# Kernel optimization log

Hardware: AMD Instinct MI355X
Metric: run time of the kernel (lower is better)

Reference implementation:

```python
import jax, jax.numpy as jnp
import numpy as np

EPS = float(np.finfo(np.float64).eps)  # np.finfo(float).eps as in torch combine


def setup_inputs() -> dict:
    key = jax.random.key(0)
    ks = jax.random.split(key, 4)
    B, E, D_in, D_h, D_out = 4096, 8, 768, 2048, 768
    return {
        "x": jax.random.normal(ks[0], (B, D_in), dtype=jnp.float32),
        "w_gate": jax.random.normal(ks[1], (D_in, E), dtype=jnp.float32) * 0.02,
        "W1": jax.random.normal(ks[2], (E, D_in, D_h), dtype=jnp.float32) * (1.0 / np.sqrt(D_in)),
        "b1": jnp.zeros((E, D_h), dtype=jnp.float32),
        "W2": jax.random.normal(ks[3], (E, D_h, D_out), dtype=jnp.float32) * (1.0 / np.sqrt(D_h)),
        "b2": jnp.zeros((E, D_out), dtype=jnp.float32),
        "k": 2,
    }


def _cv_squared(v):
    # torch .var() is unbiased (ddof=1)
    return jnp.var(v, ddof=1) / (jnp.mean(v) ** 2 + 1e-10)


def _top_k_gates(logits, k):
    B, E = logits.shape
    top_vals, top_idx = jax.lax.top_k(logits, k)        # [B, k]
    top_gates = jax.nn.softmax(top_vals, axis=1)        # softmax over the k kept logits
    gates = jnp.zeros((B, E), logits.dtype).at[jnp.arange(B)[:, None], top_idx].set(top_gates)
    return gates


def reference(x, w_gate, W1, b1, W2, b2, k):
    # --- gating (eval path: noiseless clean logits, softmax gating) ---
    logits = x @ w_gate                                  # [B, E]
    gates = _top_k_gates(logits, k)                      # [B, E], sparse (k nonzeros/row)
    # --- per-expert MLP: Linear -> gelu -> Linear -> log_softmax ---
    # Dense grouped compute over experts; gate==0 terms contribute nothing in combine.
    h = jax.nn.gelu(jnp.einsum('bi,eih->beh', x, W1) + b1[None])      # [B, E, Dh]
    lo = jax.nn.log_softmax(jnp.einsum('beh,eho->beo', h, W2) + b2[None], axis=-1)  # [B, E, Do]
    # --- combine: exp, weight by gates, scatter-add, eps-clamp, log ---
    combined = jnp.einsum('be,beo->bo', gates, jnp.exp(lo))           # [B, Do]
    y = jnp.log(jnp.where(combined == 0, EPS, combined))
    # --- load-balancing aux loss (eval: load = count of nonzero gates) ---
    importance = gates.sum(0)
    load = (gates > 0).sum(0).astype(jnp.float32)
    loss = 0.01 * (_cv_squared(importance) + _cv_squared(load))
    return y, loss
```

## Files before the change

kernel.cpp:

```cpp
#include <hip/hip_runtime.h>
#include <hip/hip_bf16.h>
#include <math.h>

typedef __hip_bfloat16 bf16;
typedef short v8s __attribute__((ext_vector_type(8)));
typedef float v4f __attribute__((ext_vector_type(4)));

#define B_TOK 4096
#define E_EXP 8
#define D_IN  768
#define D_H   2048
#define D_OUT 768
#define MAXT  72

__device__ __forceinline__ void gl_lds16(const bf16* g, bf16* l) {
  __builtin_amdgcn_global_load_lds(
      (const __attribute__((address_space(1))) unsigned int*)g,
      (__attribute__((address_space(3))) unsigned int*)l, 16, 0, 0);
}

__global__ void gate_cvt_kernel(const float* __restrict__ x, const float* __restrict__ wg,
                                bf16* __restrict__ xb,
                                float* __restrict__ gates, int* __restrict__ tidx) {
  int gt = blockIdx.x * 256 + threadIdx.x;
  int tok = gt >> 6, l = gt & 63;
  const float* xr = x + (size_t)tok * D_IN;
  bf16* xbr = xb + (size_t)tok * D_IN;
  float acc[8] = {0.f,0.f,0.f,0.f,0.f,0.f,0.f,0.f};
  #pragma unroll
  for (int i = 0; i < 3; ++i) {
    int k0 = i * 256 + l * 4;
    float4 v = *(const float4*)(xr + k0);
    union { bf16 h[4]; uint2 u; } pk;
    pk.h[0] = __float2bfloat16(v.x); pk.h[1] = __float2bfloat16(v.y);
    pk.h[2] = __float2bfloat16(v.z); pk.h[3] = __float2bfloat16(v.w);
    *(uint2*)(xbr + k0) = pk.u;
    float xv[4] = {v.x, v.y, v.z, v.w};
    #pragma unroll
    for (int j = 0; j < 4; ++j) {
      const float* wr = wg + (size_t)(k0 + j) * 8;
      float4 w0 = *(const float4*)wr;
      float4 w1 = *(const float4*)(wr + 4);
      acc[0] += xv[j] * w0.x; acc[1] += xv[j] * w0.y;
      acc[2] += xv[j] * w0.z; acc[3] += xv[j] * w0.w;
      acc[4] += xv[j] * w1.x; acc[5] += xv[j] * w1.y;
      acc[6] += xv[j] * w1.z; acc[7] += xv[j] * w1.w;
    }
  }
  #pragma unroll
  for (int d = 1; d < 64; d <<= 1)
    #pragma unroll
    for (int e = 0; e < 8; ++e) acc[e] += __shfl_xor(acc[e], d);
  if (l == 0) {
    int i1 = 0; float v1 = acc[0];
    #pragma unroll
    for (int e = 1; e < 8; ++e) if (acc[e] > v1) { v1 = acc[e]; i1 = e; }
    int i2 = -1; float v2 = -1e30f;
    #pragma unroll
    for (int e = 0; e < 8; ++e) if (e != i1 && acc[e] > v2) { v2 = acc[e]; i2 = e; }
    float ex = __expf(v2 - v1);
    float g1 = 1.f / (1.f + ex), g2 = ex / (1.f + ex);
    gates[2 * tok] = g1; gates[2 * tok + 1] = g2;
    tidx[2 * tok] = i1;  tidx[2 * tok + 1] = i2;
  }
}

__global__ void finalize_kernel(const int* __restrict__ tidx, const float* __restrict__ gates,
                                int* __restrict__ cnt_off, int* __restrict__ row_ids,
                                int* __restrict__ pos, int* __restrict__ tmap,
                                float* __restrict__ loss_out) {
  __shared__ int   hcnt[256][9];
  __shared__ float himp[256][9];
  __shared__ int   tot[8], off[8];
  __shared__ float itot[8];
  int t = threadIdx.x;
  #pragma unroll
  for (int e = 0; e < 8; ++e) { hcnt[t][e] = 0; himp[t][e] = 0.f; }
  __syncthreads();
  for (int i = 0; i < 32; ++i) {
    int idx = t * 32 + i;
    int e = tidx[idx];
    hcnt[t][e] += 1;
    himp[t][e] += gates[idx];
  }
  __syncthreads();
  if (t < 8) {
    int run = 0; float s = 0.f;
    for (int j = 0; j < 256; ++j) {
      int c = hcnt[j][t];
      hcnt[j][t] = run;
      run += c;
      s += himp[j][t];
    }
    tot[t] = run; itot[t] = s;
  }
  __syncthreads();
  if (t == 0) {
    int o = 0;
    float mi = 0.f, ml = 0.f;
    for (int e = 0; e < 8; ++e) {
      off[e] = o; o += tot[e];
      cnt_off[e] = tot[e]; cnt_off[8 + e] = off[e];
      mi += itot[e]; ml += (float)tot[e];
    }
    mi *= 0.125f; ml *= 0.125f;
    float vi = 0.f, vl = 0.f;
    for (int e = 0; e < 8; ++e) {
      float d = itot[e] - mi;        vi += d * d;
      float d2 = (float)tot[e] - ml; vl += d2 * d2;
    }
    vi /= 7.f; vl /= 7.f;
    *loss_out = 0.01f * (vi / (mi * mi + 1e-10f) + vl / (ml * ml + 1e-10f));
    int nt = 0;
    for (int e = 0; e < 8; ++e)
      for (int tt = 0; tt < (tot[e] + 127) >> 7; ++tt) {
        tmap[nt] = e; tmap[MAXT + nt] = tt; ++nt;
      }
    for (; nt < MAXT; ++nt) tmap[nt] = -1;
  }
  __syncthreads();
  for (int i = 0; i < 32; ++i) {
    int idx = t * 32 + i;
    int e = tidx[idx];
    int slot = off[e] + hcnt[t][e];
    hcnt[t][e] += 1;
    row_ids[slot] = idx >> 1;
    pos[idx] = slot;
  }
}

__global__ void transpose_cvt(const float* __restrict__ W, bf16* __restrict__ Wt,
                              int K, int N) {
  __shared__ bf16 tile[64][72];
  int e = blockIdx.z;
  int k0 = blockIdx.y * 64, n0 = blockIdx.x * 64;
  const float* Wp = W + (size_t)e * K * N;
  bf16* Wtp = Wt + (size_t)e * N * K;
  int t = threadIdx.x;
  int cr = t >> 4;
  int cc = (t & 15) * 4;
  #pragma unroll
  for (int p = 0; p < 4; ++p) {
    int kr = cr + p * 16;
    float4 v = *(const float4*)(Wp + (size_t)(k0 + kr) * N + n0 + cc);
    tile[cc + 0][kr] = __float2bfloat16(v.x);
    tile[cc + 1][kr] = __float2bfloat16(v.y);
    tile[cc + 2][kr] = __float2bfloat16(v.z);
    tile[cc + 3][kr] = __float2bfloat16(v.w);
  }
  __syncthreads();
  #pragma unroll
  for (int p = 0; p < 2; ++p) {
    int o = p * 256 + t;
    int n = o >> 3, k8 = (o & 7) * 8;
    v8s val = *(const v8s*)&tile[n][k8];
    *(v8s*)(Wtp + (size_t)(n0 + n) * K + k0 + k8) = val;
  }
}

template<int KDIM, bool GATHER, bool GELU>
__global__ __launch_bounds__(256)
void gemm_mlp(const bf16* __restrict__ Ab, const bf16* __restrict__ Wt,
              const float* __restrict__ bias, bf16* __restrict__ Outb,
              const int* __restrict__ row_ids, const int* __restrict__ cnt_off,
              const int* __restrict__ tmap, const int N) {
  constexpr int BK = 64, BM = 128, BN = 128;
  constexpr int NK = KDIM / BK;
  static_assert(NK % 2 == 0, "NK even");
  __shared__ __align__(16) bf16 lsA0[BM * BK], lsB0[BN * BK];
  __shared__ __align__(16) bf16 lsA1[BM * BK], lsB1[BN * BK];
  const int ti = blockIdx.y;
  const int e = tmap[ti];
  if (e < 0) return;
  const int rowb = tmap[MAXT + ti];
  const int cnt = cnt_off[e];
  const int off = cnt_off[8 + e];
  const int colb = blockIdx.x;
  const int t = (int)threadIdx.x, w = t >> 6, l = t & 63;
  const int cs = (l & 7) ^ (l >> 3);
  const bf16* gA[4];
  const bf16* gB[4];
  #pragma unroll
  for (int it = 0; it < 4; ++it) {
    int rt = (it * 4 + w) * 8 + (l >> 3);
    int r = rowb * BM + rt;
    int rc = r < cnt ? r : cnt - 1;
    long arow = GATHER ? (long)row_ids[off + rc] : (long)(off + rc);
    gA[it] = Ab + arow * (long)KDIM + cs * 8;
  }
  #pragma unroll
  for (int it = 0; it < 4; ++it) {
    int rt = (it * 4 + w) * 8 + (l >> 3);
    gB[it] = Wt + ((size_t)e * N + (size_t)colb * BN + rt) * KDIM + cs * 8;
  }
  v4f acc[4][4] = {};
  const int wm = w >> 1, wn = w & 1;

#define STAGE(lA, lB, k0) do {                                             \
    _Pragma("unroll")                                                      \
    for (int it = 0; it < 4; ++it) gl_lds16(gA[it] + (k0), (lA) + (it * 4 + w) * 512); \
    _Pragma("unroll")                                                      \
    for (int it = 0; it < 4; ++it) gl_lds16(gB[it] + (k0), (lB) + (it * 4 + w) * 512); \
  } while (0)

#define COMPUTE(lA, lB) do {                                               \
    _Pragma("unroll")                                                      \
    for (int kk = 0; kk < 2; ++kk) {                                       \
      v8s af[4], bfr[4];                                                   \
      _Pragma("unroll")                                                    \
      for (int fm = 0; fm < 4; ++fm) {                                     \
        int row = wm * 64 + fm * 16 + (l & 15);                            \
        int cg = kk * 4 + (l >> 4);                                        \
        af[fm] = *(const v8s*)((lA) + row * BK + ((cg ^ (row & 7)) << 3)); \
      }                                                                    \
      _Pragma("unroll")                                                    \
      for (int fn = 0; fn < 4; ++fn) {                                     \
        int row = wn * 64 + fn * 16 + (l & 15);                            \
        int cg = kk * 4 + (l >> 4);                                        \
        bfr[fn] = *(const v8s*)((lB) + row * BK + ((cg ^ (row & 7)) << 3));\
      }                                                                    \
      _Pragma("unroll")                                                    \
      for (int fm = 0; fm < 4; ++fm)                                       \
        _Pragma("unroll")                                                  \
        for (int fn = 0; fn < 4; ++fn)                                     \
          acc[fm][fn] = __builtin_amdgcn_mfma_f32_16x16x32_bf16(af[fm], bfr[fn], acc[fm][fn], 0, 0, 0); \
    }                                                                      \
  } while (0)

  STAGE(lsA0, lsB0, 0);
  __syncthreads();
  #pragma unroll 1
  for (int ks = 0; ks < NK; ks += 2) {
    if (ks + 1 < NK) STAGE(lsA1, lsB1, (ks + 1) * BK);
    COMPUTE(lsA0, lsB0);
    __syncthreads();
    if (ks + 2 < NK) STAGE(lsA0, lsB0, (ks + 2) * BK);
    COMPUTE(lsA1, lsB1);
    __syncthreads();
  }
#undef STAGE
#undef COMPUTE

  const float* bp = bias + (size_t)e * N + (size_t)colb * BN;
  #pragma unroll
  for (int fm = 0; fm < 4; ++fm) {
    int lr0 = wm * 64 + fm * 16 + (l >> 4) * 4;
    #pragma unroll
    for (int fn = 0; fn < 4; ++fn) {
      int lcol = wn * 64 + fn * 16 + (l & 15);
      float bv = bp[lcol];
      #pragma unroll
      for (int q = 0; q < 4; ++q) {
        int lr = lr0 + q;
        int r = rowb * BM + lr;
        if (r < cnt) {
          float v = acc[fm][fn][q] + bv;
          if (GELU) {
            float u = 0.7978845608028654f * (v + 0.044715f * v * v * v);
            float th = 1.f - 2.f / (__expf(2.f * u) + 1.f);
            v = 0.5f * v * (1.f + th);
          }
          Outb[(size_t)(off + r) * N + (size_t)colb * BN + lcol] = __float2bfloat16(v);
        }
      }
    }
  }
}

__global__ void combine_kernel(const bf16* __restrict__ z, const float* __restrict__ gates,
                               const int* __restrict__ pos, float* __restrict__ y) {
  int gt = blockIdx.x * 256 + threadIdx.x;
  int tok = gt >> 6, l = gt & 63;
  if (tok >= B_TOK) return;
  const bf16* z1 = z + (size_t)pos[2 * tok] * D_OUT;
  const bf16* z2 = z + (size_t)pos[2 * tok + 1] * D_OUT;
  float g1 = gates[2 * tok], g2 = gates[2 * tok + 1];
  float a[12], b[12];
  float m1 = -1e30f, m2 = -1e30f;
  #pragma unroll
  for (int i = 0; i < 12; ++i) {
    a[i] = __bfloat162float(z1[l + 64 * i]);
    b[i] = __bfloat162float(z2[l + 64 * i]);
    m1 = fmaxf(m1, a[i]); m2 = fmaxf(m2, b[i]);
  }
  #pragma unroll
  for (int d = 1; d < 64; d <<= 1) {
    m1 = fmaxf(m1, __shfl_xor(m1, d));
    m2 = fmaxf(m2, __shfl_xor(m2, d));
  }
  float s1 = 0.f, s2 = 0.f;
  #pragma unroll
  for (int i = 0; i < 12; ++i) { s1 += __expf(a[i] - m1); s2 += __expf(b[i] - m2); }
  #pragma unroll
  for (int d = 1; d < 64; d <<= 1) { s1 += __shfl_xor(s1, d); s2 += __shfl_xor(s2, d); }
  float c1 = g1 / s1, c2 = g2 / s2;
  #pragma unroll
  for (int i = 0; i < 12; ++i) {
    float cmb = c1 * __expf(a[i] - m1) + c2 * __expf(b[i] - m2);
    y[(size_t)tok * D_OUT + l + 64 * i] = logf(cmb == 0.f ? 2.2204460492503131e-16f : cmb);
  }
}

extern "C" void kernel_launch(void* const* d_in, const int* in_sizes, int n_in,
                              void* d_out, int out_size, void* d_ws, size_t ws_size,
                              hipStream_t stream) {
  const float* x  = (const float*)d_in[0];
  const float* wg = (const float*)d_in[1];
  const float* W1 = (const float*)d_in[2];
  const float* b1 = (const float*)d_in[3];
  const float* W2 = (const float*)d_in[4];
  const float* b2 = (const float*)d_in[5];
  float* out = (float*)d_out;

  char* ws = (char*)d_ws;
  int*   cnt_off = (int*)(ws + 0);
  float* gates   = (float*)(ws + 256);
  int*   tidx    = (int*)(ws + 256 + 32768);
  int*   pos     = (int*)(ws + 256 + 65536);
  int*   row_ids = (int*)(ws + 256 + 98304);
  int*   tmap    = (int*)(ws + 256 + 131072);
  const size_t base = 262144;
  bf16* x_bf = (bf16*)(ws + base);
  bf16* W1t  = (bf16*)(ws + base + 6291456);
  bf16* W2t  = (bf16*)(ws + base + 31457280);
  bf16* h_bf = (bf16*)(ws + base + 56623104);
  bf16* z_bf = (bf16*)(ws + base);

  transpose_cvt<<<dim3(D_H / 64,  D_IN / 64, E_EXP), 256, 0, stream>>>(W1, W1t, D_IN, D_H);
  transpose_cvt<<<dim3(D_OUT / 64, D_H / 64, E_EXP), 256, 0, stream>>>(W2, W2t, D_H, D_OUT);
  gate_cvt_kernel<<<dim3(1024), 256, 0, stream>>>(x, wg, x_bf, gates, tidx);
  finalize_kernel<<<dim3(1), 256, 0, stream>>>(tidx, gates, cnt_off, row_ids, pos, tmap,
                                               out + (size_t)B_TOK * D_OUT);
  gemm_mlp<D_IN, true,  true ><<<dim3(D_H / 128,  MAXT), 256, 0, stream>>>(
      x_bf, W1t, b1, h_bf, row_ids, cnt_off, tmap, D_H);
  gemm_mlp<D_H,  false, false><<<dim3(D_OUT / 128, MAXT), 256, 0, stream>>>(
      h_bf, W2t, b2, z_bf, row_ids, cnt_off, tmap, D_OUT);
  combine_kernel<<<dim3(1024), 256, 0, stream>>>(z_bf, gates, pos, out);
}
```

Before: 181.0 us.

## Deepen GEMM pipeline to four LDS stages and vectorize epilogue via LDS

Replaces the double-buffered K loop with a four-buffer ring that keeps three tiles of global-to-LDS loads in flight, using explicit vmcnt waits and raw barriers instead of __syncthreads. The epilogue now stages each warp's accumulators through LDS so each lane writes 8 contiguous bf16 values as one 16-byte store instead of scattered 2-byte stores. It aims to hide global load latency and cut store transactions. In exchange it doubles LDS use to 128 KB per block, which lowers occupancy, and depends on hand-tuned wait counts being correct.

```diff
diff --git a/kernel.cpp b/kernel.cpp
--- a/kernel.cpp
+++ b/kernel.cpp
@@ -166,9 +166,8 @@
               const int* __restrict__ tmap, const int N) {
   constexpr int BK = 64, BM = 128, BN = 128;
   constexpr int NK = KDIM / BK;
-  static_assert(NK % 2 == 0, "NK even");
-  __shared__ __align__(16) bf16 lsA0[BM * BK], lsB0[BN * BK];
-  __shared__ __align__(16) bf16 lsA1[BM * BK], lsB1[BN * BK];
+  static_assert(NK % 4 == 0, "NK multiple of 4");
+  __shared__ __align__(16) bf16 lds[4][2][BM * BK];
   const int ti = blockIdx.y;
   const int e = tmap[ti];
   if (e < 0) return;
@@ -196,72 +195,96 @@
   v4f acc[4][4] = {};
   const int wm = w >> 1, wn = w & 1;
 
-#define STAGE(lA, lB, k0) do {                                             \
-    _Pragma("unroll")                                                      \
-    for (int it = 0; it < 4; ++it) gl_lds16(gA[it] + (k0), (lA) + (it * 4 + w) * 512); \
-    _Pragma("unroll")                                                      \
-    for (int it = 0; it < 4; ++it) gl_lds16(gB[it] + (k0), (lB) + (it * 4 + w) * 512); \
+#define STAGE(b, k0) do {                                                   \
+    _Pragma("unroll")                                                       \
+    for (int it = 0; it < 4; ++it)                                          \
+      gl_lds16(gA[it] + (k0), &lds[b][0][(it * 4 + w) * 512]);              \
+    _Pragma("unroll")                                                       \
+    for (int it = 0; it < 4; ++it)                                          \
+      gl_lds16(gB[it] + (k0), &lds[b][1][(it * 4 + w) * 512]);              \
   } while (0)
 
-#define COMPUTE(lA, lB) do {                                               \
-    _Pragma("unroll")                                                      \
-    for (int kk = 0; kk < 2; ++kk) {                                       \
-      v8s af[4], bfr[4];                                                   \
-      _Pragma("unroll")                                                    \
-      for (int fm = 0; fm < 4; ++fm) {                                     \
-        int row = wm * 64 + fm * 16 + (l & 15);                            \
-        int cg = kk * 4 + (l >> 4);                                        \
-        af[fm] = *(const v8s*)((lA) + row * BK + ((cg ^ (row & 7)) << 3)); \
-      }                                                                    \
-      _Pragma("unroll")                                                    \
-      for (int fn = 0; fn < 4; ++fn) {                                     \
-        int row = wn * 64 + fn * 16 + (l & 15);                            \
-        int cg = kk * 4 + (l >> 4);                                        \
-        bfr[fn] = *(const v8s*)((lB) + row * BK + ((cg ^ (row & 7)) << 3));\
-      }                                                                    \
-      _Pragma("unroll")                                                    \
-      for (int fm = 0; fm < 4; ++fm)                                       \
-        _Pragma("unroll")                                                  \
-        for (int fn = 0; fn < 4; ++fn)                                     \
+#define COMPUTE(b) do {                                                     \
+    _Pragma("unroll")                                                       \
+    for (int kk = 0; kk < 2; ++kk) {                                        \
+      v8s af[4], bfr[4];                                                    \
+      _Pragma("unroll")                                                     \
+      for (int fm = 0; fm < 4; ++fm) {                                      \
+        int row = wm * 64 + fm * 16 + (l & 15);                             \
+        int cg = kk * 4 + (l >> 4);                                         \
+        af[fm] = *(const v8s*)(&lds[b][0][0] + row * BK + ((cg ^ (row & 7)) << 3)); \
+      }                                                                     \
+      _Pragma("unroll")                                                     \
+      for (int fn = 0; fn < 4; ++fn) {                                      \
+        int row = wn * 64 + fn * 16 + (l & 15);                             \
+        int cg = kk * 4 + (l >> 4);                                         \
+        bfr[fn] = *(const v8s*)(&lds[b][1][0] + row * BK + ((cg ^ (row & 7)) << 3)); \
+      }                                                                     \
+      _Pragma("unroll")                                                     \
+      for (int fm = 0; fm < 4; ++fm)                                        \
+        _Pragma("unroll")                                                   \
+        for (int fn = 0; fn < 4; ++fn)                                      \
           acc[fm][fn] = __builtin_amdgcn_mfma_f32_16x16x32_bf16(af[fm], bfr[fn], acc[fm][fn], 0, 0, 0); \
-    }                                                                      \
+    }                                                                       \
   } while (0)
 
-  STAGE(lsA0, lsB0, 0);
-  __syncthreads();
+#define PIPE_STEP(j, kn, VMS) do {                                          \
+    if ((kn) < NK) STAGE((j + 3) & 3, (kn) * BK);                           \
+    asm volatile("s_waitcnt " VMS ::: "memory");                            \
+    __builtin_amdgcn_sched_barrier(0);                                      \
+    __builtin_amdgcn_s_barrier();                                           \
+    __builtin_amdgcn_sched_barrier(0);                                      \
+    COMPUTE(j);                                                             \
+    __builtin_amdgcn_s_barrier();                                           \
+    __builtin_amdgcn_sched_barrier(0);                                      \
+  } while (0)
+
+  STAGE(0, 0); STAGE(1, BK); STAGE(2, 2 * BK);
   #pragma unroll 1
-  for (int ks = 0; ks < NK; ks += 2) {
-    if (ks + 1 < NK) STAGE(lsA1, lsB1, (ks + 1) * BK);
-    COMPUTE(lsA0, lsB0);
-    __syncthreads();
-    if (ks + 2 < NK) STAGE(lsA0, lsB0, (ks + 2) * BK);
-    COMPUTE(lsA1, lsB1);
-    __syncthreads();
-  }
+  for (int i4 = 0; i4 < NK - 4; i4 += 4) {
+    PIPE_STEP(0, i4 + 3, "vmcnt(24)");
+    PIPE_STEP(1, i4 + 4, "vmcnt(24)");
+    PIPE_STEP(2, i4 + 5, "vmcnt(24)");
+    PIPE_STEP(3, i4 + 6, "vmcnt(24)");
+  }
+  PIPE_STEP(0, NK - 1, "vmcnt(24)");
+  PIPE_STEP(1, NK,     "vmcnt(16)");
+  PIPE_STEP(2, NK + 1, "vmcnt(8)");
+  PIPE_STEP(3, NK + 2, "vmcnt(0)");
 #undef STAGE
 #undef COMPUTE
-
-  const float* bp = bias + (size_t)e * N + (size_t)colb * BN;
+#undef PIPE_STEP
+
+  float* eps = (float*)(&lds[0][0][0]) + w * (16 * 68);
+  const float* bp = bias + (size_t)e * N + (size_t)colb * BN + wn * 64 + (l & 7) * 8;
+  float bv[8];
+  #pragma unroll
+  for (int jj = 0; jj < 8; ++jj) bv[jj] = bp[jj];
   #pragma unroll
   for (int fm = 0; fm < 4; ++fm) {
-    int lr0 = wm * 64 + fm * 16 + (l >> 4) * 4;
-    #pragma unroll
-    for (int fn = 0; fn < 4; ++fn) {
-      int lcol = wn * 64 + fn * 16 + (l & 15);
-      float bv = bp[lcol];
+    #pragma unroll
+    for (int fn = 0; fn < 4; ++fn)
       #pragma unroll
-      for (int q = 0; q < 4; ++q) {
-        int lr = lr0 + q;
-        int r = rowb * BM + lr;
-        if (r < cnt) {
-          float v = acc[fm][fn][q] + bv;
+      for (int q = 0; q < 4; ++q)
+        eps[((l >> 4) * 4 + q) * 68 + fn * 16 + (l & 15)] = acc[fm][fn][q];
+    #pragma unroll
+    for (int half = 0; half < 2; ++half) {
+      int row = (l >> 3) + 8 * half;
+      int r = rowb * BM + wm * 64 + fm * 16 + row;
+      if (r < cnt) {
+        const float* rp = eps + row * 68 + (l & 7) * 8;
+        union { bf16 h[8]; uint4 u; } pk;
+        #pragma unroll
+        for (int jj = 0; jj < 8; ++jj) {
+          float v = rp[jj] + bv[jj];
           if (GELU) {
             float u = 0.7978845608028654f * (v + 0.044715f * v * v * v);
             float th = 1.f - 2.f / (__expf(2.f * u) + 1.f);
             v = 0.5f * v * (1.f + th);
           }
-          Outb[(size_t)(off + r) * N + (size_t)colb * BN + lcol] = __float2bfloat16(v);
+          pk.h[jj] = __float2bfloat16(v);
         }
+        *(uint4*)(Outb + (size_t)(off + r) * N + (size_t)colb * BN + wn * 64 + (l & 7) * 8) = pk.u;
       }
     }
   }
```

Measured after the change: 177.3 us. 1.02x faster.
